# Optimization experiments

Hardware: AMD Instinct MI355X
Metric: run time of the kernel (lower is better)

## Reference

```python
import jax, jax.numpy as jnp
import numpy as np

N_NODES = 100000
HID = 128
N_EDGES = 600000


def sage_conv(h, src, dst, Wl, bl, Wr, n_nodes):
    # PyG SAGEConv (mean aggr): out = lin_l(mean_{j->i} h_j) + lin_r(h_i)
    msgs = h[src]                                               # [E, d] gather
    agg = jax.ops.segment_sum(msgs, dst, num_segments=n_nodes)  # [N, d]
    cnt = jax.ops.segment_sum(jnp.ones((src.shape[0], 1), h.dtype), dst,
                              num_segments=n_nodes)             # [N, 1]
    mean = agg / jnp.maximum(cnt, 1.0)                          # isolated nodes -> 0
    return mean @ Wl.T + bl + h @ Wr.T


def setup_inputs() -> dict:
    key = jax.random.key(0)
    ks = jax.random.split(key, 8)
    scale = 1.0 / np.sqrt(HID)
    x = jnp.arange(N_NODES, dtype=jnp.int64) if jax.config.jax_enable_x64 else jnp.arange(N_NODES, dtype=jnp.int32)
    edge_index = jax.random.randint(ks[0], (2, N_EDGES), 0, N_NODES)
    emb = jax.random.normal(ks[1], (N_NODES, HID), dtype=jnp.float32) * scale
    Wl1 = jax.random.normal(ks[2], (HID, HID), dtype=jnp.float32) * scale
    bl1 = jnp.zeros((HID,), jnp.float32)
    Wr1 = jax.random.normal(ks[3], (HID, HID), dtype=jnp.float32) * scale
    Wl2 = jax.random.normal(ks[4], (HID, HID), dtype=jnp.float32) * scale
    bl2 = jnp.zeros((HID,), jnp.float32)
    Wr2 = jax.random.normal(ks[5], (HID, HID), dtype=jnp.float32) * scale
    return {"x": x, "edge_index": edge_index, "emb": emb,
            "Wl1": Wl1, "bl1": bl1, "Wr1": Wr1,
            "Wl2": Wl2, "bl2": bl2, "Wr2": Wr2}


def reference(x, edge_index, emb, Wl1, bl1, Wr1, Wl2, bl2, Wr2):
    src, dst = edge_index[0], edge_index[1]
    n = emb.shape[0]
    h = emb[x]                                          # embedding lookup [N, d]
    h = jax.nn.relu(sage_conv(h, src, dst, Wl1, bl1, Wr1, n))  # dropout = eval identity
    h = jax.nn.relu(sage_conv(h, src, dst, Wl2, bl2, Wr2, n))
    return h
```

## Files before the change

### kernel.cpp

```cpp
#include <hip/hip_runtime.h>

#define HID 128

typedef unsigned short ushort_t;
typedef unsigned int uint_t;
typedef float f32x4 __attribute__((ext_vector_type(4)));
typedef short s16x8 __attribute__((ext_vector_type(8)));

__device__ __forceinline__ ushort_t f2bf(float f) {
  uint_t u = __float_as_uint(f);
  uint_t r = (u + 0x7FFFu + ((u >> 16) & 1u)) >> 16;
  return (ushort_t)r;
}
__device__ __forceinline__ float bfLo(uint_t v) { return __uint_as_float(v << 16); }
__device__ __forceinline__ float bfHi(uint_t v) { return __uint_as_float(v & 0xFFFF0000u); }

__device__ __forceinline__ uint4 pack8(const float4& lo, const float4& hi) {
  uint4 p;
  p.x = (uint_t)f2bf(lo.x) | ((uint_t)f2bf(lo.y) << 16);
  p.y = (uint_t)f2bf(lo.z) | ((uint_t)f2bf(lo.w) << 16);
  p.z = (uint_t)f2bf(hi.x) | ((uint_t)f2bf(hi.y) << 16);
  p.w = (uint_t)f2bf(hi.z) | ((uint_t)f2bf(hi.w) << 16);
  return p;
}

__global__ __launch_bounds__(256) void prep_kernel(
    const float* __restrict__ emb, const int* __restrict__ x,
    ushort_t* __restrict__ hb, int N,
    const float* __restrict__ Wl1, const float* __restrict__ Wr1,
    const float* __restrict__ Wl2, const float* __restrict__ Wr2,
    ushort_t* __restrict__ wsw,
    const int* __restrict__ dst, int* __restrict__ deg, int E) {
  int tid = blockIdx.x * 256 + threadIdx.x;
  const int eN = (N + 7) >> 3;
  int gthreads = eN * 16;
  if (tid < gthreads) {
    int r0 = tid >> 4, j = (tid & 15) * 8;
    int rs[8], si[8];
#pragma unroll
    for (int k = 0; k < 8; k++) {
      int r = r0 + k * eN;
      rs[k] = r;
      int rc = (r < N) ? r : N - 1;
      si[k] = x[rc];
    }
    float4 lo[8], hi[8];
#pragma unroll
    for (int k = 0; k < 8; k++) {
      const float* pk = &emb[(size_t)si[k] * HID + j];
      lo[k] = *(const float4*)pk;
      hi[k] = *(const float4*)(pk + 4);
    }
#pragma unroll
    for (int k = 0; k < 8; k++) {
      if (rs[k] < N)
        *(uint4*)&hb[(size_t)rs[k] * HID + j] = pack8(lo[k], hi[k]);
    }
    return;
  }
  tid -= gthreads;
  if (tid < 65536) {
    const float* srcs[4] = {Wl1, Wr1, Wl2, Wr2};
    int m = tid >> 14, idx = tid & 16383;
    int j = idx & 7;
    int lane = (idx >> 3) & 63;
    int nt = (idx >> 9) & 7;
    int ks = (idx >> 12) & 3;
    int row = nt * 16 + (lane & 15);
    int col = ks * 32 + (lane >> 4) * 8 + j;
    wsw[tid] = f2bf(srcs[m][row * HID + col]);
    return;
  }
  tid -= 65536;
  if (tid < E) atomicAdd(&deg[dst[tid]], 1);
}

__global__ __launch_bounds__(256) void scan1_kernel(
    const int* __restrict__ deg, int* __restrict__ offsets,
    int* __restrict__ sums, int N) {
  __shared__ int s[256];
  int b = blockIdx.x, t = threadIdx.x;
  int base = b * 1024 + t * 4;
  int v0 = 0, v1 = 0, v2 = 0, v3 = 0;
  if (base + 0 < N) v0 = deg[base + 0];
  if (base + 1 < N) v1 = deg[base + 1];
  if (base + 2 < N) v2 = deg[base + 2];
  if (base + 3 < N) v3 = deg[base + 3];
  int mySum = v0 + v1 + v2 + v3;
  s[t] = mySum;
  __syncthreads();
  for (int off = 1; off < 256; off <<= 1) {
    int v = (t >= off) ? s[t - off] : 0;
    __syncthreads();
    s[t] += v;
    __syncthreads();
  }
  int excl = s[t] - mySum;
  if (t == 255) sums[b] = s[255];
  if (base + 0 < N) offsets[base + 0] = excl;
  if (base + 1 < N) offsets[base + 1] = excl + v0;
  if (base + 2 < N) offsets[base + 2] = excl + v0 + v1;
  if (base + 3 < N) offsets[base + 3] = excl + v0 + v1 + v2;
}

__global__ __launch_bounds__(256) void scan3_kernel(
    int* __restrict__ offsets, const int* __restrict__ sums,
    int* __restrict__ cursor, int N, int E, int nb) {
  __shared__ int red[256];
  int t = threadIdx.x;
  int chunk = (blockIdx.x * 256) >> 10;
  red[t] = (t < chunk) ? sums[t] : 0;
  __syncthreads();
  for (int off = 128; off > 0; off >>= 1) {
    if (t < off) red[t] += red[t + off];
    __syncthreads();
  }
  int prefix = red[0];
  int i = blockIdx.x * 256 + t;
  if (i < N) {
    int v = offsets[i] + prefix;
    offsets[i] = v;
    cursor[i] = v;
  } else if (i == N) {
    offsets[N] = E;
  }
}

__global__ __launch_bounds__(256) void fill_kernel(
    const int* __restrict__ src, const int* __restrict__ dst,
    int* __restrict__ cursor, int* __restrict__ csr, int E) {
  int e = blockIdx.x * 256 + threadIdx.x;
  if (e >= E) return;
  int d = dst[e];
  int pos = atomicAdd(&cursor[d], 1);
  csr[pos] = src[e];
}

__global__ __launch_bounds__(256) void aggregate_kernel(
    const ushort_t* __restrict__ hb, const int* __restrict__ offsets,
    const int* __restrict__ csr, ushort_t* __restrict__ meanb, int N) {
  int t = threadIdx.x;
  int node = blockIdx.x * 16 + (t >> 4);
  if (node >= N) return;
  int l15 = t & 15;
  int o0 = offsets[node], o1 = offsets[node + 1];
  int last = o1 - 1;

  float acc[8];
#pragma unroll
  for (int i = 0; i < 8; i++) acc[i] = 0.f;

  for (int e = o0; e < o1; e += 8) {
    uint4 v[8];
    float m[8];
#pragma unroll
    for (int i = 0; i < 8; i++) {
      int idx = e + i;
      bool val = idx < o1;
      int sidx = csr[val ? idx : last];
      v[i] = *(const uint4*)&hb[(size_t)sidx * HID + l15 * 8];
      m[i] = val ? 1.f : 0.f;
    }
#pragma unroll
    for (int i = 0; i < 8; i++) {
      acc[0] = fmaf(m[i], bfLo(v[i].x), acc[0]);
      acc[1] = fmaf(m[i], bfHi(v[i].x), acc[1]);
      acc[2] = fmaf(m[i], bfLo(v[i].y), acc[2]);
      acc[3] = fmaf(m[i], bfHi(v[i].y), acc[3]);
      acc[4] = fmaf(m[i], bfLo(v[i].z), acc[4]);
      acc[5] = fmaf(m[i], bfHi(v[i].z), acc[5]);
      acc[6] = fmaf(m[i], bfLo(v[i].w), acc[6]);
      acc[7] = fmaf(m[i], bfHi(v[i].w), acc[7]);
    }
  }

  int d = o1 - o0;
  float inv = 1.0f / (float)(d > 1 ? d : 1);
  uint4 p;
  p.x = (uint_t)f2bf(acc[0] * inv) | ((uint_t)f2bf(acc[1] * inv) << 16);
  p.y = (uint_t)f2bf(acc[2] * inv) | ((uint_t)f2bf(acc[3] * inv) << 16);
  p.z = (uint_t)f2bf(acc[4] * inv) | ((uint_t)f2bf(acc[5] * inv) << 16);
  p.w = (uint_t)f2bf(acc[6] * inv) | ((uint_t)f2bf(acc[7] * inv) << 16);
  *(uint4*)&meanb[(size_t)node * HID + l15 * 8] = p;
}

__global__ __launch_bounds__(256) void mfma_gemm_kernel(
    const ushort_t* __restrict__ meanb, const ushort_t* __restrict__ hb,
    const ushort_t* __restrict__ WlS, const ushort_t* __restrict__ WrS,
    const float* __restrict__ bias, float* __restrict__ outF,
    ushort_t* __restrict__ outB, int N, int outIsBf16) {
  __shared__ ushort_t ws[32768];
  const int t = threadIdx.x;
  const int wave = t >> 6;
  const int lane = t & 63;
  const int tileBase = (blockIdx.x * 4 + wave) * 64;
  const int l15 = lane & 15;
  const int quad = lane >> 4;
  const int kq = quad * 8;

  s16x8 a[2][2][2][4];
#pragma unroll
  for (int tl = 0; tl < 2; tl++) {
    int rb = tileBase + tl * 32;
    if (rb >= N) break;
    int r0 = rb + l15;       if (r0 >= N) r0 = N - 1;
    int r1 = rb + 16 + l15;  if (r1 >= N) r1 = N - 1;
#pragma unroll
    for (int ks = 0; ks < 4; ks++) {
      a[tl][0][0][ks] = *(const s16x8*)&meanb[(size_t)r0 * HID + ks * 32 + kq];
      a[tl][0][1][ks] = *(const s16x8*)&meanb[(size_t)r1 * HID + ks * 32 + kq];
      a[tl][1][0][ks] = *(const s16x8*)&hb[(size_t)r0 * HID + ks * 32 + kq];
      a[tl][1][1][ks] = *(const s16x8*)&hb[(size_t)r1 * HID + ks * 32 + kq];
    }
  }

#pragma unroll
  for (int it = 0; it < 8; it++) {
    int o = (it * 256 + t) * 8;
    *(s16x8*)&ws[o] = *(const s16x8*)&WlS[o];
    *(s16x8*)&ws[16384 + o] = *(const s16x8*)&WrS[o];
  }
  __syncthreads();

#pragma unroll
  for (int tl = 0; tl < 2; tl++) {
    int rowBase = tileBase + tl * 32;
    if (rowBase >= N) break;

    f32x4 acc[2][8];
#pragma unroll
    for (int mt = 0; mt < 2; mt++)
#pragma unroll
      for (int nt = 0; nt < 8; nt++) acc[mt][nt] = (f32x4){0.f, 0.f, 0.f, 0.f};

#pragma unroll
    for (int half = 0; half < 2; half++) {
      const int hbase = half * 16384;
#pragma unroll
      for (int ks = 0; ks < 4; ks++)
#pragma unroll
        for (int nt = 0; nt < 8; nt++) {
          s16x8 bfrag = *(const s16x8*)&ws[hbase + ((ks * 8 + nt) * 64 + lane) * 8];
          acc[0][nt] = __builtin_amdgcn_mfma_f32_16x16x32_bf16(a[tl][half][0][ks], bfrag, acc[0][nt], 0, 0, 0);
          acc[1][nt] = __builtin_amdgcn_mfma_f32_16x16x32_bf16(a[tl][half][1][ks], bfrag, acc[1][nt], 0, 0, 0);
        }
    }

#pragma unroll
    for (int mt = 0; mt < 2; mt++) {
#pragma unroll
      for (int nt = 0; nt < 8; nt++) {
        int col = nt * 16 + l15;
        float bv = bias[col];
#pragma unroll
        for (int r = 0; r < 4; r++) {
          int row = rowBase + mt * 16 + quad * 4 + r;
          if (row < N) {
            float v = fmaxf(acc[mt][nt][r] + bv, 0.f);
            if (outIsBf16) outB[(size_t)row * HID + col] = f2bf(v);
            else           outF[(size_t)row * HID + col] = v;
          }
        }
      }
    }
  }
}

extern "C" void kernel_launch(void* const* d_in, const int* in_sizes, int n_in,
                              void* d_out, int out_size, void* d_ws, size_t ws_size,
                              hipStream_t stream) {
  const int* x = (const int*)d_in[0];
  const int* ei = (const int*)d_in[1];
  const float* emb = (const float*)d_in[2];
  const float* Wl1 = (const float*)d_in[3];
  const float* bl1 = (const float*)d_in[4];
  const float* Wr1 = (const float*)d_in[5];
  const float* Wl2 = (const float*)d_in[6];
  const float* bl2 = (const float*)d_in[7];
  const float* Wr2 = (const float*)d_in[8];
  float* out = (float*)d_out;

  const int N = in_sizes[0];
  const int E = in_sizes[1] / 2;
  const int* srcI = ei;
  const int* dstI = ei + E;

  char* p = (char*)d_ws;
  ushort_t* hb = (ushort_t*)p;    p += (size_t)N * HID * sizeof(ushort_t);
  ushort_t* hb2 = (ushort_t*)p;   p += (size_t)N * HID * sizeof(ushort_t);
  ushort_t* meanb = (ushort_t*)p; p += (size_t)N * HID * sizeof(ushort_t);
  ushort_t* wb = (ushort_t*)p;    p += (size_t)4 * 16384 * sizeof(ushort_t);
  int* deg = (int*)p;             p += (size_t)((N + 3) & ~3) * sizeof(int);
  int* offsets = (int*)p;         p += (size_t)((N + 4) & ~3) * sizeof(int);
  int* cursor = (int*)p;          p += (size_t)((N + 3) & ~3) * sizeof(int);
  int* csr = (int*)p;             p += (size_t)((E + 3) & ~3) * sizeof(int);
  int* sums = (int*)p;            p += 256 * sizeof(int);

  ushort_t* Wlb1 = wb;
  ushort_t* Wrb1 = wb + 16384;
  ushort_t* Wlb2 = wb + 32768;
  ushort_t* Wrb2 = wb + 49152;

  const int nScanBlocks = (N + 1023) / 1024;
  const int eBlocks = (E + 255) / 256;
  const int gemmBlocks = (N + 255) / 256;
  const int aggBlocks = (N + 15) / 16;
  const int eN = (N + 7) / 8;
  const int prepBlocks = (eN * 16 + 65536 + E + 255) / 256;

  hipMemsetAsync(deg, 0, (size_t)N * sizeof(int), stream);
  prep_kernel<<<prepBlocks, 256, 0, stream>>>(emb, x, hb, N,
                                              Wl1, Wr1, Wl2, Wr2, wb,
                                              dstI, deg, E);
  scan1_kernel<<<nScanBlocks, 256, 0, stream>>>(deg, offsets, sums, N);
  scan3_kernel<<<(N + 256) / 256, 256, 0, stream>>>(offsets, sums, cursor,
                                                    N, E, nScanBlocks);
  fill_kernel<<<eBlocks, 256, 0, stream>>>(srcI, dstI, cursor, csr, E);

  aggregate_kernel<<<aggBlocks, 256, 0, stream>>>(hb, offsets, csr, meanb, N);
  mfma_gemm_kernel<<<gemmBlocks, 256, 0, stream>>>(meanb, hb, Wlb1, Wrb1, bl1,
                                                   nullptr, hb2, N, 1);

  aggregate_kernel<<<aggBlocks, 256, 0, stream>>>(hb2, offsets, csr, meanb, N);
  mfma_gemm_kernel<<<gemmBlocks, 256, 0, stream>>>(meanb, hb2, Wlb2, Wrb2, bl2,
                                                   out, nullptr, N, 0);
}
```

Baseline: 311.5 us.

## Remap blocks to contiguous per-XCD regions and halve GEMM rows per block

```diff
diff --git a/kernel.cpp b/kernel.cpp
--- a/kernel.cpp
+++ b/kernel.cpp
@@ -14,6 +14,12 @@
 }
 __device__ __forceinline__ float bfLo(uint_t v) { return __uint_as_float(v << 16); }
 __device__ __forceinline__ float bfHi(uint_t v) { return __uint_as_float(v & 0xFFFF0000u); }
+
+__device__ __forceinline__ int xcd_region(int b, int nwg) {
+  int q = nwg >> 3, r = nwg & 7;
+  int x = b & 7, i = b >> 3;
+  return x * q + (x < r ? x : r) + i;
+}
 
 __device__ __forceinline__ uint4 pack8(const float4& lo, const float4& hi) {
   uint4 p;
@@ -140,7 +146,8 @@
     const ushort_t* __restrict__ hb, const int* __restrict__ offsets,
     const int* __restrict__ csr, ushort_t* __restrict__ meanb, int N) {
   int t = threadIdx.x;
-  int node = blockIdx.x * 16 + (t >> 4);
+  int rIdx = xcd_region(blockIdx.x, gridDim.x);
+  int node = rIdx * 16 + (t >> 4);
   if (node >= N) return;
   int l15 = t & 15;
   int o0 = offsets[node], o1 = offsets[node + 1];
@@ -193,24 +200,24 @@
   const int t = threadIdx.x;
   const int wave = t >> 6;
   const int lane = t & 63;
-  const int tileBase = (blockIdx.x * 4 + wave) * 64;
+  const int rIdx = xcd_region(blockIdx.x, gridDim.x);
+  const int rowBase = (rIdx * 4 + wave) * 32;
   const int l15 = lane & 15;
   const int quad = lane >> 4;
   const int kq = quad * 8;
-
-  s16x8 a[2][2][2][4];
-#pragma unroll
-  for (int tl = 0; tl < 2; tl++) {
-    int rb = tileBase + tl * 32;
-    if (rb >= N) break;
-    int r0 = rb + l15;       if (r0 >= N) r0 = N - 1;
-    int r1 = rb + 16 + l15;  if (r1 >= N) r1 = N - 1;
+  const bool active = rowBase < N;
+
+  int r0 = rowBase + l15;       if (r0 >= N) r0 = N - 1;
+  int r1 = rowBase + 16 + l15;  if (r1 >= N) r1 = N - 1;
+
+  s16x8 a[2][2][4];
+  if (active) {
 #pragma unroll
     for (int ks = 0; ks < 4; ks++) {
-      a[tl][0][0][ks] = *(const s16x8*)&meanb[(size_t)r0 * HID + ks * 32 + kq];
-      a[tl][0][1][ks] = *(const s16x8*)&meanb[(size_t)r1 * HID + ks * 32 + kq];
-      a[tl][1][0][ks] = *(const s16x8*)&hb[(size_t)r0 * HID + ks * 32 + kq];
-      a[tl][1][1][ks] = *(const s16x8*)&hb[(size_t)r1 * HID + ks * 32 + kq];
+      a[0][0][ks] = *(const s16x8*)&meanb[(size_t)r0 * HID + ks * 32 + kq];
+      a[0][1][ks] = *(const s16x8*)&meanb[(size_t)r1 * HID + ks * 32 + kq];
+      a[1][0][ks] = *(const s16x8*)&hb[(size_t)r0 * HID + ks * 32 + kq];
+      a[1][1][ks] = *(const s16x8*)&hb[(size_t)r1 * HID + ks * 32 + kq];
     }
   }
 
@@ -222,11 +229,7 @@
   }
   __syncthreads();
 
-#pragma unroll
-  for (int tl = 0; tl < 2; tl++) {
-    int rowBase = tileBase + tl * 32;
-    if (rowBase >= N) break;
-
+  if (active) {
     f32x4 acc[2][8];
 #pragma unroll
     for (int mt = 0; mt < 2; mt++)
@@ -241,8 +244,8 @@
 #pragma unroll
         for (int nt = 0; nt < 8; nt++) {
           s16x8 bfrag = *(const s16x8*)&ws[hbase + ((ks * 8 + nt) * 64 + lane) * 8];
-          acc[0][nt] = __builtin_amdgcn_mfma_f32_16x16x32_bf16(a[tl][half][0][ks], bfrag, acc[0][nt], 0, 0, 0);
-          acc[1][nt] = __builtin_amdgcn_mfma_f32_16x16x32_bf16(a[tl][half][1][ks], bfrag, acc[1][nt], 0, 0, 0);
+          acc[0][nt] = __builtin_amdgcn_mfma_f32_16x16x32_bf16(a[half][0][ks], bfrag, acc[0][nt], 0, 0, 0);
+          acc[1][nt] = __builtin_amdgcn_mfma_f32_16x16x32_bf16(a[half][1][ks], bfrag, acc[1][nt], 0, 0, 0);
         }
     }
 
@@ -303,7 +306,7 @@
 
   const int nScanBlocks = (N + 1023) / 1024;
   const int eBlocks = (E + 255) / 256;
-  const int gemmBlocks = (N + 255) / 256;
+  const int gemmBlocks = (N + 127) / 128;
   const int aggBlocks = (N + 15) / 16;
   const int eN = (N + 7) / 8;
   const int prepBlocks = (eN * 16 + 65536 + E + 255) / 256;
```

After: 285.7 us. -8.3%, faster.
